# Kernel optimization log

Hardware: AMD Instinct MI355X
Metric: run time of the kernel (lower is better)

Reference implementation:

```python
import jax, jax.numpy as jnp
import numpy as np

N1, N2, D = 256, 256, 1024


def setup_inputs() -> dict:
    key = jax.random.key(0)
    k1, k2, k3, k4, k5, k6, k7 = jax.random.split(key, 7)
    return {
        "features1": jax.random.normal(k1, (N1, D), dtype=jnp.float32),
        "features2": jax.random.normal(k2, (N2, D), dtype=jnp.float32),
        "mask_cross": jax.random.randint(k3, (N1, N2), 0, 2, dtype=jnp.int32),
        "mask1": jax.random.randint(k4, (N1, N1), 0, 2, dtype=jnp.int32),
        "mask2": jax.random.randint(k5, (N2, N2), 0, 2, dtype=jnp.int32),
        "mask_sents1": jax.random.randint(k6, (N1,), 0, 2, dtype=jnp.int32).astype(bool),
        "mask_sents2": jax.random.randint(k7, (N2,), 0, 2, dtype=jnp.int32).astype(bool),
    }


def _compute_loss(sim, mask, sel):
    # sim: [R, C] similarities; mask: [R, C] in {0,1}; sel: [R] row selector in {0,1}.
    # Torch code masked-selects rows (mask_sents) and pos/neg entries per row, then
    # sums -logsigmoid(sim_pos - sim_neg) over all (pos, neg) pairs. Rows with zero
    # pos or zero neg contribute 0 loss and 0 pairs, so the data-dependent branch is
    # exactly reproduced by multiplicative masking.
    mp = mask * sel[:, None]          # selected positive mask [R, C]
    mn = 1.0 - mask                   # negative mask [R, C]
    # -logsigmoid(x) == softplus(-x)
    nls = jax.nn.softplus(-(sim[:, :, None] - sim[:, None, :]))  # [R, C, C]
    loss = jnp.einsum('ij,ik,ijk->', mp, mn, nls)
    pair_num = jnp.sum(mp.sum(axis=1) * mn.sum(axis=1) * sel)
    return loss, pair_num


def reference(features1, features2, mask_cross, mask1, mask2, mask_sents1, mask_sents2):
    # sim_type == 'dot': no normalization; temperature is unused by the math.
    mc = mask_cross.astype(jnp.float32)
    m1 = mask1.astype(jnp.float32)
    m2 = mask2.astype(jnp.float32)
    s1 = mask_sents1.astype(jnp.float32)
    s2 = mask_sents2.astype(jnp.float32)

    sim12 = features1 @ features2.T   # [N1, N2]
    sim11 = features1 @ features1.T   # [N1, N1]
    sim22 = features2 @ features2.T   # [N2, N2]

    l1, p1 = _compute_loss(sim12, mc, s1)
    l2, p2 = _compute_loss(sim12.T, mc.T, s2)
    l3, p3 = _compute_loss(sim11, m1, s1)
    l4, p4 = _compute_loss(sim22, m2, s2)

    loss = l1 + l2 + l3 + l4
    pair_num = p1 + p2 + p3 + p4
    return jnp.where(pair_num > 0, loss / jnp.maximum(pair_num, 1.0), loss)
```

## Files before the change

### kernel.cpp

```cpp
#include <hip/hip_runtime.h>
#include <hip/hip_bf16.h>
#include <math.h>


#define NN 256
#define DD 1024

typedef __attribute__((ext_vector_type(8))) short short8;
typedef __attribute__((ext_vector_type(4))) float f32x4;

__device__ __forceinline__ unsigned short f32_to_bf16_rne(float x) {
    unsigned int u = __float_as_uint(x);
    u += 0x7fffu + ((u >> 16) & 1u);
    return (unsigned short)(u >> 16);
}

__global__ __launch_bounds__(256) void convert_prep_kernel(
        const float* __restrict__ f1, const float* __restrict__ f2,
        unsigned short* __restrict__ b1, unsigned short* __restrict__ b2,
        const void* ms1, const void* ms2,
        float* sel1, float* sel2,
        double* lossAcc, unsigned long long* pairAcc) {
    const int bid = blockIdx.x;
    const int tid = threadIdx.x;
    if (bid < 512) {
        const float* src = (bid < 256) ? f1 : f2;
        unsigned short* dst = (bid < 256) ? b1 : b2;
        int base = ((bid & 255) * 256 + tid) * 4;
        float4 v = *(const float4*)(src + base);
        ushort4 o;
        o.x = f32_to_bf16_rne(v.x);
        o.y = f32_to_bf16_rne(v.y);
        o.z = f32_to_bf16_rne(v.z);
        o.w = f32_to_bf16_rne(v.w);
        *(ushort4*)(dst + base) = o;
    } else {
        __shared__ int nz1, nz2;
        if (tid == 0) { nz1 = 0; nz2 = 0; }
        __syncthreads();
        const unsigned char* c1 = (const unsigned char*)ms1;
        const unsigned char* c2 = (const unsigned char*)ms2;
        if ((tid & 3) != 0) {
            if (c1[tid] != 0) atomicOr(&nz1, 1);
            if (c2[tid] != 0) atomicOr(&nz2, 1);
        }
        __syncthreads();
        sel1[tid] = (nz1 != 0) ? (c1[tid] ? 1.0f : 0.0f)
                               : (float)((const int*)ms1)[tid];
        sel2[tid] = (nz2 != 0) ? (c2[tid] ? 1.0f : 0.0f)
                               : (float)((const int*)ms2)[tid];
        if (tid == 0) { *lossAcc = 0.0; *pairAcc = 0ULL; }
    }
}

__global__ __launch_bounds__(256) void gemm_mfma(
        const unsigned short* __restrict__ b1,
        const unsigned short* __restrict__ b2,
        float* __restrict__ sims) {
    const int gwave = blockIdx.x * 4 + (threadIdx.x >> 6);
    const int m = gwave >> 8;
    const int t = gwave & 255;
    const int tr = t >> 4, tc = t & 15;
    const unsigned short* A  = (m == 2) ? b2 : b1;
    const unsigned short* Bm = (m == 0) ? b2 : ((m == 1) ? b1 : b2);
    float* C = sims + m * (NN * NN);

    const int lane = threadIdx.x & 63;
    const int r = lane & 15;
    const int quad = lane >> 4;

    const unsigned short* aptr = A  + (tr * 16 + r) * DD + quad * 8;
    const unsigned short* bptr = Bm + (tc * 16 + r) * DD + quad * 8;

    f32x4 acc = {0.f, 0.f, 0.f, 0.f};
#pragma unroll 8
    for (int k0 = 0; k0 < DD; k0 += 32) {
        short8 af = *(const short8*)(aptr + k0);
        short8 bf = *(const short8*)(bptr + k0);
        acc = __builtin_amdgcn_mfma_f32_16x16x32_bf16(af, bf, acc, 0, 0, 0);
    }
    const int row0 = tr * 16 + quad * 4;
    const int col = tc * 16 + (lane & 15);
#pragma unroll
    for (int rr = 0; rr < 4; rr++) {
        C[(row0 + rr) * NN + col] = acc[rr];
    }
}

__global__ __launch_bounds__(256) void loss_kernel(
        const float* __restrict__ sims,
        const int* __restrict__ mc,
        const int* __restrict__ m1,
        const int* __restrict__ m2,
        const float* __restrict__ sel1,
        const float* __restrict__ sel2,
        double* lossAcc, unsigned long long* pairAcc) {
    const int i = blockIdx.x;
    const int c = blockIdx.y;
    const int tid = threadIdx.x;

    const float* sim12 = sims;
    const float* sim11 = sims + NN * NN;
    const float* sim22 = sims + 2 * NN * NN;

    float sel, simv;
    int maskv;
    if (c == 0) {
        sel = sel1[i]; simv = sim12[i * NN + tid]; maskv = mc[i * NN + tid];
    } else if (c == 1) {
        sel = sel2[i]; simv = sim12[tid * NN + i]; maskv = mc[tid * NN + i];
    } else if (c == 2) {
        sel = sel1[i]; simv = sim11[i * NN + tid]; maskv = m1[i * NN + tid];
    } else {
        sel = sel2[i]; simv = sim22[i * NN + tid]; maskv = m2[i * NN + tid];
    }
    if (sel == 0.0f) return;

    const float LOG2E = 1.4426950408889634f;
    const float LN2   = 0.6931471805599453f;

    __shared__ float sPos[NN];
    __shared__ float sNeg[NN];
    __shared__ int wcnt[4];
    __shared__ float red[4];

    const int lane = tid & 63;
    const int w = tid >> 6;
    const bool pos = (maskv != 0);
    unsigned long long bal = __ballot(pos);
    if (lane == 0) wcnt[w] = __popcll(bal);
    __syncthreads();

    int posBase = 0, np_ = 0;
#pragma unroll
    for (int q = 0; q < 4; q++) {
        int v = wcnt[q];
        if (q < w) posBase += v;
        np_ += v;
    }
    const int nn_ = NN - np_;

    const unsigned long long ltmask = (1ull << lane) - 1ull;
    const int pp = __popcll(bal & ltmask);
    const float tval = simv * LOG2E;
    if (pos) sPos[posBase + pp] = tval;
    else     sNeg[(w * 64 - posBase) + (lane - pp)] = tval;
    __syncthreads();

    if (np_ == 0 || nn_ == 0) return;
    if (tid == 0) atomicAdd(pairAcc, (unsigned long long)(np_ * nn_));

    const float tn = (tid < nn_) ? sNeg[tid] : -1e30f;
    float accL = 0.f, accM = 0.f;
    for (int jj = 0; jj < np_; jj++) {
        float sp = sPos[jj];
        float x2 = tn - sp;
        float e = __builtin_amdgcn_exp2f(-fabsf(x2));
        accL += __builtin_amdgcn_logf(1.0f + e);
        accM += fmaxf(x2, 0.0f);
    }
    float local = (accL + accM) * LN2;

#pragma unroll
    for (int off = 32; off > 0; off >>= 1) local += __shfl_down(local, off, 64);
    if (lane == 0) red[w] = local;
    __syncthreads();
    if (tid == 0) {
        double bsum = (double)red[0] + (double)red[1] +
                      (double)red[2] + (double)red[3];
        atomicAdd(lossAcc, bsum);
    }
}

__global__ void finalize_kernel(const double* lossAcc,
                                const unsigned long long* pairAcc,
                                float* out) {
    double loss = *lossAcc;
    unsigned long long p = *pairAcc;
    double r = (p > 0ULL) ? (loss / (double)p) : loss;
    out[0] = (float)r;
}

extern "C" void kernel_launch(void* const* d_in, const int* in_sizes, int n_in,
                              void* d_out, int out_size, void* d_ws, size_t ws_size,
                              hipStream_t stream) {
    const float* f1 = (const float*)d_in[0];
    const float* f2 = (const float*)d_in[1];
    const int* mc = (const int*)d_in[2];
    const int* m1 = (const int*)d_in[3];
    const int* m2 = (const int*)d_in[4];
    const void* ms1 = d_in[5];
    const void* ms2 = d_in[6];

    char* ws = (char*)d_ws;
    float* sims          = (float*)ws;
    unsigned short* b1   = (unsigned short*)(ws + 786432);
    unsigned short* b2   = (unsigned short*)(ws + 1310720);
    float* sel1          = (float*)(ws + 1835008);
    float* sel2          = (float*)(ws + 1836032);
    double* lossAcc      = (double*)(ws + 1837056);
    unsigned long long* pairAcc = (unsigned long long*)(ws + 1837064);

    convert_prep_kernel<<<513, 256, 0, stream>>>(f1, f2, b1, b2, ms1, ms2,
                                                 sel1, sel2, lossAcc, pairAcc);
    gemm_mfma<<<192, 256, 0, stream>>>(b1, b2, sims);
    loss_kernel<<<dim3(256, 4), 256, 0, stream>>>(sims, mc, m1, m2, sel1, sel2,
                                                  lossAcc, pairAcc);
    finalize_kernel<<<1, 1, 0, stream>>>(lossAcc, pairAcc, (float*)d_out);
}
```

Before: 92.18 us.

## Fuse bf16 conversion into GEMM, drop atomics for per-block partials

The separate fp32-to-bf16 conversion/prep kernel is removed. The GEMM now loads fp32 features directly and converts them in registers before the MFMA. Mask-selector decoding moves into the loss kernel, and global atomics are replaced by per-block partial loss and count arrays that a parallel 256-thread finalize kernel reduces. The inner softplus loop is unrolled by four with float4 LDS reads and padded sentinels. This removes one launch and the intermediate bf16 buffers, at the cost of the GEMM reading twice as many bytes and each loss block redundantly re-detecting the mask format.

New measurement: 96.35 us. +4.5%, slower.

```diff
diff --git a/kernel.cpp b/kernel.cpp
--- a/kernel.cpp
+++ b/kernel.cpp
@@ -15,72 +15,50 @@
     return (unsigned short)(u >> 16);
 }
 
-__global__ __launch_bounds__(256) void convert_prep_kernel(
+__device__ __forceinline__ short8 cvt8(float4 a, float4 b) {
+    short8 r;
+    r[0] = (short)f32_to_bf16_rne(a.x);
+    r[1] = (short)f32_to_bf16_rne(a.y);
+    r[2] = (short)f32_to_bf16_rne(a.z);
+    r[3] = (short)f32_to_bf16_rne(a.w);
+    r[4] = (short)f32_to_bf16_rne(b.x);
+    r[5] = (short)f32_to_bf16_rne(b.y);
+    r[6] = (short)f32_to_bf16_rne(b.z);
+    r[7] = (short)f32_to_bf16_rne(b.w);
+    return r;
+}
+
+__global__ __launch_bounds__(256) void gemm_mfma(
         const float* __restrict__ f1, const float* __restrict__ f2,
-        unsigned short* __restrict__ b1, unsigned short* __restrict__ b2,
-        const void* ms1, const void* ms2,
-        float* sel1, float* sel2,
-        double* lossAcc, unsigned long long* pairAcc) {
-    const int bid = blockIdx.x;
-    const int tid = threadIdx.x;
-    if (bid < 512) {
-        const float* src = (bid < 256) ? f1 : f2;
-        unsigned short* dst = (bid < 256) ? b1 : b2;
-        int base = ((bid & 255) * 256 + tid) * 4;
-        float4 v = *(const float4*)(src + base);
-        ushort4 o;
-        o.x = f32_to_bf16_rne(v.x);
-        o.y = f32_to_bf16_rne(v.y);
-        o.z = f32_to_bf16_rne(v.z);
-        o.w = f32_to_bf16_rne(v.w);
-        *(ushort4*)(dst + base) = o;
-    } else {
-        __shared__ int nz1, nz2;
-        if (tid == 0) { nz1 = 0; nz2 = 0; }
-        __syncthreads();
-        const unsigned char* c1 = (const unsigned char*)ms1;
-        const unsigned char* c2 = (const unsigned char*)ms2;
-        if ((tid & 3) != 0) {
-            if (c1[tid] != 0) atomicOr(&nz1, 1);
-            if (c2[tid] != 0) atomicOr(&nz2, 1);
-        }
-        __syncthreads();
-        sel1[tid] = (nz1 != 0) ? (c1[tid] ? 1.0f : 0.0f)
-                               : (float)((const int*)ms1)[tid];
-        sel2[tid] = (nz2 != 0) ? (c2[tid] ? 1.0f : 0.0f)
-                               : (float)((const int*)ms2)[tid];
-        if (tid == 0) { *lossAcc = 0.0; *pairAcc = 0ULL; }
-    }
-}
-
-__global__ __launch_bounds__(256) void gemm_mfma(
-        const unsigned short* __restrict__ b1,
-        const unsigned short* __restrict__ b2,
         float* __restrict__ sims) {
     const int gwave = blockIdx.x * 4 + (threadIdx.x >> 6);
     const int m = gwave >> 8;
     const int t = gwave & 255;
     const int tr = t >> 4, tc = t & 15;
-    const unsigned short* A  = (m == 2) ? b2 : b1;
-    const unsigned short* Bm = (m == 0) ? b2 : ((m == 1) ? b1 : b2);
+    const float* A  = (m == 2) ? f2 : f1;
+    const float* Bm = (m == 0) ? f2 : ((m == 1) ? f1 : f2);
     float* C = sims + m * (NN * NN);
 
     const int lane = threadIdx.x & 63;
     const int r = lane & 15;
     const int quad = lane >> 4;
 
-    const unsigned short* aptr = A  + (tr * 16 + r) * DD + quad * 8;
-    const unsigned short* bptr = Bm + (tc * 16 + r) * DD + quad * 8;
+    const float* aptr = A  + (tr * 16 + r) * DD + quad * 8;
+    const float* bptr = Bm + (tc * 16 + r) * DD + quad * 8;
 
     f32x4 acc = {0.f, 0.f, 0.f, 0.f};
-#pragma unroll 8
+#pragma unroll 4
     for (int k0 = 0; k0 < DD; k0 += 32) {
-        short8 af = *(const short8*)(aptr + k0);
-        short8 bf = *(const short8*)(bptr + k0);
+        float4 a0 = *(const float4*)(aptr + k0);
+        float4 a1 = *(const float4*)(aptr + k0 + 4);
+        float4 b0 = *(const float4*)(bptr + k0);
+        float4 b1 = *(const float4*)(bptr + k0 + 4);
+        short8 af = cvt8(a0, a1);
+        short8 bf = cvt8(b0, b1);
         acc = __builtin_amdgcn_mfma_f32_16x16x32_bf16(af, bf, acc, 0, 0, 0);
     }
     const int row0 = tr * 16 + quad * 4;
-    const int col = tc * 16 + (lane & 15);
+    const int col = tc * 16 + r;
 #pragma unroll
     for (int rr = 0; rr < 4; rr++) {
         C[(row0 + rr) * NN + col] = acc[rr];
@@ -92,40 +70,56 @@
         const int* __restrict__ mc,
         const int* __restrict__ m1,
         const int* __restrict__ m2,
-        const float* __restrict__ sel1,
-        const float* __restrict__ sel2,
-        double* lossAcc, unsigned long long* pairAcc) {
+        const void* ms1, const void* ms2,
+        float* __restrict__ pLoss, int* __restrict__ pCnt) {
     const int i = blockIdx.x;
     const int c = blockIdx.y;
     const int tid = threadIdx.x;
+    const int bid = c * NN + i;
+    const int lane = tid & 63;
+    const int w = tid >> 6;
 
     const float* sim12 = sims;
     const float* sim11 = sims + NN * NN;
     const float* sim22 = sims + 2 * NN * NN;
 
-    float sel, simv;
-    int maskv;
-    if (c == 0) {
-        sel = sel1[i]; simv = sim12[i * NN + tid]; maskv = mc[i * NN + tid];
-    } else if (c == 1) {
-        sel = sel2[i]; simv = sim12[tid * NN + i]; maskv = mc[tid * NN + i];
-    } else if (c == 2) {
-        sel = sel1[i]; simv = sim11[i * NN + tid]; maskv = m1[i * NN + tid];
-    } else {
-        sel = sel2[i]; simv = sim22[i * NN + tid]; maskv = m2[i * NN + tid];
-    }
-    if (sel == 0.0f) return;
-
-    const float LOG2E = 1.4426950408889634f;
-    const float LN2   = 0.6931471805599453f;
-
-    __shared__ float sPos[NN];
+    __shared__ alignas(16) float sPos[NN + 4];
     __shared__ float sNeg[NN];
     __shared__ int wcnt[4];
     __shared__ float red[4];
-
-    const int lane = tid & 63;
-    const int w = tid >> 6;
+    __shared__ int detFlag;
+
+    const void* ms = (c == 1 || c == 3) ? ms2 : ms1;
+    if (tid == 0) detFlag = 0;
+    __syncthreads();
+    const unsigned char* mb = (const unsigned char*)ms;
+    bool nzb = ((tid & 3) != 0) && (mb[tid] != 0);
+    unsigned long long det = __ballot(nzb);
+    if (lane == 0 && det) atomicOr(&detFlag, 1);
+
+    float simv;
+    int maskv;
+    if (c == 0) {
+        simv = sim12[i * NN + tid]; maskv = mc[i * NN + tid];
+    } else if (c == 1) {
+        simv = sim12[tid * NN + i]; maskv = mc[tid * NN + i];
+    } else if (c == 2) {
+        simv = sim11[i * NN + tid]; maskv = m1[i * NN + tid];
+    } else {
+        simv = sim22[i * NN + tid]; maskv = m2[i * NN + tid];
+    }
+    __syncthreads();
+    const bool isBool = (detFlag != 0);
+    const float sel = isBool ? (mb[i] ? 1.0f : 0.0f)
+                             : (float)((const int*)ms)[i];
+    if (sel == 0.0f) {
+        if (tid == 0) { pLoss[bid] = 0.0f; pCnt[bid] = 0; }
+        return;
+    }
+
+    const float LOG2E = 1.4426950408889634f;
+    const float LN2   = 0.6931471805599453f;
+
     const bool pos = (maskv != 0);
     unsigned long long bal = __ballot(pos);
     if (lane == 0) wcnt[w] = __popcll(bal);
@@ -145,40 +139,71 @@
     const float tval = simv * LOG2E;
     if (pos) sPos[posBase + pp] = tval;
     else     sNeg[(w * 64 - posBase) + (lane - pp)] = tval;
-    __syncthreads();
-
-    if (np_ == 0 || nn_ == 0) return;
-    if (tid == 0) atomicAdd(pairAcc, (unsigned long long)(np_ * nn_));
-
+    if (tid < 4) sPos[np_ + tid] = 1e30f;
+    __syncthreads();
+
+    if (np_ == 0 || nn_ == 0) {
+        if (tid == 0) { pLoss[bid] = 0.0f; pCnt[bid] = 0; }
+        return;
+    }
+
+    const int np4 = (np_ + 3) & ~3;
     const float tn = (tid < nn_) ? sNeg[tid] : -1e30f;
-    float accL = 0.f, accM = 0.f;
-    for (int jj = 0; jj < np_; jj++) {
-        float sp = sPos[jj];
-        float x2 = tn - sp;
-        float e = __builtin_amdgcn_exp2f(-fabsf(x2));
-        accL += __builtin_amdgcn_logf(1.0f + e);
-        accM += fmaxf(x2, 0.0f);
-    }
-    float local = (accL + accM) * LN2;
+    float accL0 = 0.f, accM0 = 0.f, accL1 = 0.f, accM1 = 0.f;
+    for (int jj = 0; jj < np4; jj += 4) {
+        float4 sp = *(const float4*)&sPos[jj];
+        float x0 = tn - sp.x;
+        float x1 = tn - sp.y;
+        float x2 = tn - sp.z;
+        float x3 = tn - sp.w;
+        accL0 += __builtin_amdgcn_logf(1.0f + __builtin_amdgcn_exp2f(-fabsf(x0)));
+        accM0 += fmaxf(x0, 0.0f);
+        accL1 += __builtin_amdgcn_logf(1.0f + __builtin_amdgcn_exp2f(-fabsf(x1)));
+        accM1 += fmaxf(x1, 0.0f);
+        accL0 += __builtin_amdgcn_logf(1.0f + __builtin_amdgcn_exp2f(-fabsf(x2)));
+        accM0 += fmaxf(x2, 0.0f);
+        accL1 += __builtin_amdgcn_logf(1.0f + __builtin_amdgcn_exp2f(-fabsf(x3)));
+        accM1 += fmaxf(x3, 0.0f);
+    }
+    float local = ((accL0 + accL1) + (accM0 + accM1)) * LN2;
 
 #pragma unroll
     for (int off = 32; off > 0; off >>= 1) local += __shfl_down(local, off, 64);
     if (lane == 0) red[w] = local;
     __syncthreads();
     if (tid == 0) {
-        double bsum = (double)red[0] + (double)red[1] +
-                      (double)red[2] + (double)red[3];
-        atomicAdd(lossAcc, bsum);
-    }
-}
-
-__global__ void finalize_kernel(const double* lossAcc,
-                                const unsigned long long* pairAcc,
-                                float* out) {
-    double loss = *lossAcc;
-    unsigned long long p = *pairAcc;
-    double r = (p > 0ULL) ? (loss / (double)p) : loss;
-    out[0] = (float)r;
+        pLoss[bid] = red[0] + red[1] + red[2] + red[3];
+        pCnt[bid] = np_ * nn_;
+    }
+}
+
+__global__ __launch_bounds__(256) void finalize_kernel(
+        const float* __restrict__ pLoss, const int* __restrict__ pCnt,
+        float* __restrict__ out) {
+    const int tid = threadIdx.x;
+    const int lane = tid & 63;
+    double s = 0.0;
+    long long cnt = 0;
+#pragma unroll
+    for (int q = 0; q < 4; q++) {
+        int k = tid + q * 256;
+        s += (double)pLoss[k];
+        cnt += (long long)pCnt[k];
+    }
+#pragma unroll
+    for (int off = 32; off > 0; off >>= 1) {
+        s += __shfl_down(s, off, 64);
+        cnt += __shfl_down(cnt, off, 64);
+    }
+    __shared__ double rs[4];
+    __shared__ long long rc[4];
+    if (lane == 0) { rs[tid >> 6] = s; rc[tid >> 6] = cnt; }
+    __syncthreads();
+    if (tid == 0) {
+        double loss = rs[0] + rs[1] + rs[2] + rs[3];
+        long long p = rc[0] + rc[1] + rc[2] + rc[3];
+        out[0] = (float)((p > 0) ? loss / (double)p : loss);
+    }
 }
 
 extern "C" void kernel_launch(void* const* d_in, const int* in_sizes, int n_in,
@@ -193,18 +218,12 @@
     const void* ms2 = d_in[6];
 
     char* ws = (char*)d_ws;
-    float* sims          = (float*)ws;
-    unsigned short* b1   = (unsigned short*)(ws + 786432);
-    unsigned short* b2   = (unsigned short*)(ws + 1310720);
-    float* sel1          = (float*)(ws + 1835008);
-    float* sel2          = (float*)(ws + 1836032);
-    double* lossAcc      = (double*)(ws + 1837056);
-    unsigned long long* pairAcc = (unsigned long long*)(ws + 1837064);
-
-    convert_prep_kernel<<<513, 256, 0, stream>>>(f1, f2, b1, b2, ms1, ms2,
-                                                 sel1, sel2, lossAcc, pairAcc);
-    gemm_mfma<<<192, 256, 0, stream>>>(b1, b2, sims);
-    loss_kernel<<<dim3(256, 4), 256, 0, stream>>>(sims, mc, m1, m2, sel1, sel2,
-                                                  lossAcc, pairAcc);
-    finalize_kernel<<<1, 1, 0, stream>>>(lossAcc, pairAcc, (float*)d_out);
-}
+    float* sims  = (float*)ws;
+    float* pLoss = (float*)(ws + 786432);
+    int*   pCnt  = (int*)(ws + 790528);
+
+    gemm_mfma<<<192, 256, 0, stream>>>(f1, f2, sims);
+    loss_kernel<<<dim3(256, 4), 256, 0, stream>>>(sims, mc, m1, m2, ms1, ms2,
+                                                  pLoss, pCnt);
+    finalize_kernel<<<1, 256, 0, stream>>>(pLoss, pCnt, (float*)d_out);
+}
```
